# Performance work log

Measured on AMD Instinct MI355X. Metric: run time of the kernel, lower is better.

## Reference

```python
import jax, jax.numpy as jnp
import numpy as np

N = 8192
HIDDEN = 1024
PROJ = 128
T = 0.07
LN_EPS = 1e-12


def _neg_indices(n):
    # Static [n, n-2] index matrix: for row i, all j except j==i and the
    # paired sample j == (i + n//2) % n. Computed with numpy (n is static).
    half = n // 2
    idx = np.arange(n)
    mask = np.ones((n, n), dtype=bool)
    mask[idx, idx] = False
    mask[idx, (idx + half) % n] = False
    return np.nonzero(mask)[1].reshape(n, n - 2)


def setup_inputs() -> dict:
    key = jax.random.key(0)
    ks = jax.random.split(key, 3)
    scale = 1.0 / np.sqrt(HIDDEN)
    return {
        "x": jax.random.normal(ks[0], (N, HIDDEN), dtype=jnp.float32),
        "dense_w": jax.random.normal(ks[1], (HIDDEN, HIDDEN), dtype=jnp.float32) * scale,
        "dense_b": jnp.zeros((HIDDEN,), dtype=jnp.float32),
        "ln_gamma": jnp.ones((HIDDEN,), dtype=jnp.float32),
        "ln_beta": jnp.zeros((HIDDEN,), dtype=jnp.float32),
        "dec_w": jax.random.normal(ks[2], (HIDDEN, PROJ), dtype=jnp.float32) * scale,
        "dec_b": jnp.zeros((PROJ,), dtype=jnp.float32),
    }


def reference(x, dense_w, dense_b, ln_gamma, ln_beta, dec_w, dec_b):
    # dense -> gelu (exact, erf-based as in BERT) -> layernorm -> decoder
    h = x @ dense_w + dense_b
    h = jax.nn.gelu(h, approximate=False)
    mu = jnp.mean(h, axis=-1, keepdims=True)
    var = jnp.mean(jnp.square(h - mu), axis=-1, keepdims=True)
    h = (h - mu) * jax.lax.rsqrt(var + LN_EPS) * ln_gamma + ln_beta
    z = h @ dec_w + dec_b  # [N, 128]

    n = z.shape[0]
    half = n // 2
    # positive logit: dot(z_i, z_partner)
    l_pos = jnp.sum(z[:half] * z[half:], axis=-1)  # [N/2]
    l_pos = jnp.concatenate([l_pos, l_pos])[:, None]  # [N, 1]

    # full similarity matrix, then gather the N-2 negatives per row
    sims = z @ z.T  # [N, N]
    neg_idx = jnp.asarray(_neg_indices(n))  # static [N, N-2]
    l_neg = jnp.take_along_axis(sims, neg_idx, axis=1)  # [N, N-2]

    logits = jnp.concatenate([l_pos, l_neg], axis=1) / T  # [N, N-1]
    # CrossEntropyLoss with labels == 0
    loss = jnp.mean(jax.nn.logsumexp(logits, axis=-1) - logits[:, 0])
    return loss
```

## Files before the change

### kernel.cpp

```cpp
#include <hip/hip_runtime.h>
#include <math.h>
#include <stdint.h>

#define NN 8192
#define HID 1024
#define PROJ 128

constexpr float INV_T = 1.0f / 0.07f;
constexpr float LN_EPS = 1e-12f;
constexpr float CC = 14.285714285714286f * 1.4426950408889634f;

typedef __bf16 bf16x8 __attribute__((ext_vector_type(8)));
typedef float f32x4 __attribute__((ext_vector_type(4)));

#define EXP2(x) __builtin_amdgcn_exp2f(x)

#define GLD16(g, l)                                                     \
  __builtin_amdgcn_global_load_lds(                                     \
      (const __attribute__((address_space(1))) uint32_t*)(g),           \
      (__attribute__((address_space(3))) uint32_t*)(l), 16, 0, 0)

__device__ __forceinline__ uint16_t f2bf(float f) {
  union { float f; uint32_t u; } c; c.f = f;
  uint32_t r = (c.u + 0x7FFFu + ((c.u >> 16) & 1u)) >> 16;
  return (uint16_t)r;
}
__device__ __forceinline__ float bf2f(uint16_t u) {
  union { uint32_t u; float f; } c; c.u = ((uint32_t)u) << 16;
  return c.f;
}

__device__ __forceinline__ float gelu_f(float v) {
  float w = v * v;
  float u = v * fmaf(w, 0.0356774081f, 0.7978845608f);
  float e = EXP2(u * -2.8853900818f);
  return v * __builtin_amdgcn_rcpf(1.0f + e);
}

__global__ __launch_bounds__(256) void k_conv(const float* __restrict__ in,
                                              uint16_t* __restrict__ out) {
  int i = (blockIdx.x * 256 + threadIdx.x) * 4;
  float4 v = *(const float4*)(in + i);
  ushort4 o;
  o.x = f2bf(v.x); o.y = f2bf(v.y); o.z = f2bf(v.z); o.w = f2bf(v.w);
  *(ushort4*)(out + i) = o;
}

__global__ __launch_bounds__(256) void k_transpose(const float* __restrict__ in,
                                                   uint16_t* __restrict__ out,
                                                   int R, int C) {
  __shared__ uint16_t t[32][33];
  const int cb = blockIdx.x * 32, rb = blockIdx.y * 32;
  const int tr = threadIdx.x >> 3, tc4 = (threadIdx.x & 7) * 4;
  float4 v = *(const float4*)(in + (size_t)(rb + tr) * C + cb + tc4);
  t[tc4 + 0][tr] = f2bf(v.x);
  t[tc4 + 1][tr] = f2bf(v.y);
  t[tc4 + 2][tr] = f2bf(v.z);
  t[tc4 + 3][tr] = f2bf(v.w);
  __syncthreads();
  const int oc = threadIdx.x >> 3, or4 = (threadIdx.x & 7) * 4;
  ushort4 o;
  o.x = t[oc][or4 + 0]; o.y = t[oc][or4 + 1];
  o.z = t[oc][or4 + 2]; o.w = t[oc][or4 + 3];
  *(ushort4*)(out + (size_t)(cb + oc) * R + rb + or4) = o;
}

__global__ __launch_bounds__(256) void k_gemm1(
    const uint16_t* __restrict__ Ab, const uint16_t* __restrict__ Bt,
    const float* __restrict__ bias, uint16_t* __restrict__ Hout) {
  __shared__ __align__(16) uint16_t As[64 * 32];
  __shared__ __align__(16) uint16_t Bs[128 * 32];
  const int tid = threadIdx.x;
  const int bn = blockIdx.x * 128, bm = blockIdx.y * 64;
  const int wave = tid >> 6, lane = tid & 63;
  const int wx = wave & 1, wy = wave >> 1;
  const int col = lane & 15, quad = lane >> 4;
  f32x4 acc[2][4] = {};
  const char* Abase = (const char*)Ab;
  const char* Bbase = (const char*)Bt;
  for (int k0 = 0; k0 < HID; k0 += 32) {
    __syncthreads();
    {
      int off = tid * 16;
      int row = off >> 6, inner = off & 63;
      GLD16(Abase + ((size_t)(bm + row) * HID + k0) * 2 + inner,
            (char*)As + off);
    }
#pragma unroll
    for (int l = 0; l < 2; ++l) {
      int off = tid * 16 + l * 4096;
      int row = off >> 6, inner = off & 63;
      GLD16(Bbase + ((size_t)(bn + row) * HID + k0) * 2 + inner,
            (char*)Bs + off);
    }
    __syncthreads();
    bf16x8 a[2], b[4];
#pragma unroll
    for (int mt = 0; mt < 2; ++mt)
      a[mt] = *(const bf16x8*)&As[(wy * 32 + mt * 16 + col) * 32 + quad * 8];
#pragma unroll
    for (int nt = 0; nt < 4; ++nt)
      b[nt] = *(const bf16x8*)&Bs[(wx * 64 + nt * 16 + col) * 32 + quad * 8];
#pragma unroll
    for (int mt = 0; mt < 2; ++mt)
#pragma unroll
      for (int nt = 0; nt < 4; ++nt)
        acc[mt][nt] = __builtin_amdgcn_mfma_f32_16x16x32_bf16(
            a[mt], b[nt], acc[mt][nt], 0, 0, 0);
  }
#pragma unroll
  for (int nt = 0; nt < 4; ++nt) {
    int gj = bn + wx * 64 + nt * 16 + col;
    float bv = bias[gj];
#pragma unroll
    for (int mt = 0; mt < 2; ++mt)
#pragma unroll
      for (int r = 0; r < 4; ++r) {
        int gi = bm + wy * 32 + mt * 16 + quad * 4 + r;
        Hout[(size_t)gi * HID + gj] = f2bf(gelu_f(acc[mt][nt][r] + bv));
      }
  }
}

__global__ __launch_bounds__(256) void k_layernorm(
    uint16_t* __restrict__ Hm, const float* __restrict__ gamma,
    const float* __restrict__ beta) {
  const int row = blockIdx.x;
  const int tid = threadIdx.x;
  uint16_t* hr = Hm + (size_t)row * HID;
  ushort4 u = *(const ushort4*)(hr + tid * 4);
  float f0 = bf2f(u.x), f1 = bf2f(u.y), f2 = bf2f(u.z), f3 = bf2f(u.w);
  float sum = f0 + f1 + f2 + f3;
  float sq = f0 * f0 + f1 * f1 + f2 * f2 + f3 * f3;
#pragma unroll
  for (int off = 32; off > 0; off >>= 1) {
    sum += __shfl_down(sum, off);
    sq += __shfl_down(sq, off);
  }
  __shared__ float rs[4], rq[4];
  __shared__ float mu_s, rstd_s;
  const int wave = tid >> 6, lane = tid & 63;
  if (lane == 0) { rs[wave] = sum; rq[wave] = sq; }
  __syncthreads();
  if (tid == 0) {
    float s = rs[0] + rs[1] + rs[2] + rs[3];
    float q = rq[0] + rq[1] + rq[2] + rq[3];
    float mu = s * (1.0f / HID);
    float var = q * (1.0f / HID) - mu * mu;
    mu_s = mu;
    rstd_s = rsqrtf(var + LN_EPS);
  }
  __syncthreads();
  const float mu = mu_s, r = rstd_s;
  float4 g = *(const float4*)(gamma + tid * 4);
  float4 b = *(const float4*)(beta + tid * 4);
  ushort4 o;
  o.x = f2bf((f0 - mu) * r * g.x + b.x);
  o.y = f2bf((f1 - mu) * r * g.y + b.y);
  o.z = f2bf((f2 - mu) * r * g.z + b.z);
  o.w = f2bf((f3 - mu) * r * g.w + b.w);
  *(ushort4*)(hr + tid * 4) = o;
}

__global__ __launch_bounds__(256) void k_gemm2(
    const uint16_t* __restrict__ Hn, const uint16_t* __restrict__ Wt2,
    const float* __restrict__ bd, uint16_t* __restrict__ Z) {
  __shared__ __align__(16) uint16_t As2[32 * 32];
  __shared__ __align__(16) uint16_t Bs2[128 * 32];
  const int tid = threadIdx.x;
  const int bm = blockIdx.x * 32;
  const int wave = tid >> 6, lane = tid & 63;
  const int wx = wave & 1, wy = wave >> 1;
  const int col = lane & 15, quad = lane >> 4;
  f32x4 acc[4] = {};
  const char* Abase = (const char*)Hn;
  const char* Bbase = (const char*)Wt2;
  for (int k0 = 0; k0 < HID; k0 += 32) {
    __syncthreads();
    if (tid < 128) {
      int off = tid * 16;
      int row = off >> 6, inner = off & 63;
      GLD16(Abase + ((size_t)(bm + row) * HID + k0) * 2 + inner,
            (char*)As2 + off);
    }
#pragma unroll
    for (int l = 0; l < 2; ++l) {
      int off = tid * 16 + l * 4096;
      int row = off >> 6, inner = off & 63;
      GLD16(Bbase + ((size_t)row * HID + k0) * 2 + inner, (char*)Bs2 + off);
    }
    __syncthreads();
    bf16x8 a = *(const bf16x8*)&As2[(wy * 16 + col) * 32 + quad * 8];
#pragma unroll
    for (int nt = 0; nt < 4; ++nt) {
      bf16x8 b = *(const bf16x8*)&Bs2[(wx * 64 + nt * 16 + col) * 32 + quad * 8];
      acc[nt] = __builtin_amdgcn_mfma_f32_16x16x32_bf16(a, b, acc[nt], 0, 0, 0);
    }
  }
#pragma unroll
  for (int nt = 0; nt < 4; ++nt) {
    int gj = wx * 64 + nt * 16 + col;
    float bv = bd[gj];
#pragma unroll
    for (int r = 0; r < 4; ++r) {
      int gi = bm + wy * 16 + quad * 4 + r;
      Z[(size_t)gi * PROJ + gj] = f2bf(acc[nt][r] + bv);
    }
  }
}

__device__ __forceinline__ void lse_update(float& m, float& s, float v0,
                                           float v1, float v2, float v3) {
  float lm = fmaxf(fmaxf(v0, v1), fmaxf(v2, v3));
  float mn = fmaxf(m, lm);
  float t = mn * CC;
  s = s * EXP2(m * CC - t) + EXP2(v0 * CC - t) + EXP2(v1 * CC - t) +
      EXP2(v2 * CC - t) + EXP2(v3 * CC - t);
  m = mn;
}

__global__ __launch_bounds__(256) void k_sim(const uint16_t* __restrict__ Z,
                                             float* __restrict__ m_part,
                                             float* __restrict__ s_part,
                                             float* __restrict__ pos_arr) {
  __shared__ __align__(16) uint16_t Zj[128 * 136];
  const int tid = threadIdx.x;
  const int bi = blockIdx.x * 64;
  const int chunk = blockIdx.y;
  const int wave = tid >> 6, lane = tid & 63;
  const int wx = wave & 1, wy = wave >> 1;
  const int col = lane & 15, quad = lane >> 4;

  bf16x8 afr[2][4];
#pragma unroll
  for (int mt = 0; mt < 2; ++mt)
#pragma unroll
    for (int kc = 0; kc < 4; ++kc)
      afr[mt][kc] = *(const bf16x8*)(Z +
          (size_t)(bi + wy * 32 + mt * 16 + col) * PROJ + kc * 32 + quad * 8);

  float mrow[8], srow[8];
#pragma unroll
  for (int i = 0; i < 8; ++i) { mrow[i] = -INFINITY; srow[i] = 0.f; }

  const int jbase = chunk * 512;
  for (int t = 0; t < 4; ++t) {
    const int j0 = jbase + t * 128;
    __syncthreads();
#pragma unroll
    for (int l = 0; l < 8; ++l) {
      int idx = tid + l * 256;
      int row = idx >> 4, kq = (idx & 15) * 8;
      *(uint4*)&Zj[row * 136 + kq] =
          *(const uint4*)(Z + (size_t)(j0 + row) * PROJ + kq);
    }
    __syncthreads();
    f32x4 acc[2][4] = {};
#pragma unroll
    for (int kc = 0; kc < 4; ++kc) {
      bf16x8 b[4];
#pragma unroll
      for (int nt = 0; nt < 4; ++nt)
        b[nt] = *(const bf16x8*)&Zj[(wx * 64 + nt * 16 + col) * 136 +
                                    kc * 32 + quad * 8];
#pragma unroll
      for (int mt = 0; mt < 2; ++mt)
#pragma unroll
        for (int nt = 0; nt < 4; ++nt)
          acc[mt][nt] = __builtin_amdgcn_mfma_f32_16x16x32_bf16(
              afr[mt][kc], b[nt], acc[mt][nt], 0, 0, 0);
    }
    const bool is_diag = (j0 == (bi & ~127));
    const bool is_pos = (j0 == (((bi + NN / 2) & (NN - 1)) & ~127));
    if (!(is_diag || is_pos)) {
#pragma unroll
      for (int mt = 0; mt < 2; ++mt)
#pragma unroll
        for (int r = 0; r < 4; ++r)
          lse_update(mrow[mt * 4 + r], srow[mt * 4 + r], acc[mt][0][r],
                     acc[mt][1][r], acc[mt][2][r], acc[mt][3][r]);
    } else {
#pragma unroll
      for (int mt = 0; mt < 2; ++mt)
#pragma unroll
        for (int r = 0; r < 4; ++r) {
          int gi = bi + wy * 32 + mt * 16 + quad * 4 + r;
          int partner = (gi + NN / 2) & (NN - 1);
          float v[4];
#pragma unroll
          for (int nt = 0; nt < 4; ++nt) {
            int gj = j0 + wx * 64 + nt * 16 + col;
            float d = acc[mt][nt][r];
            if (is_pos && gj == partner) pos_arr[gi] = d;
            v[nt] = (is_diag && gj == gi) ? -INFINITY : d;
          }
          lse_update(mrow[mt * 4 + r], srow[mt * 4 + r], v[0], v[1], v[2],
                     v[3]);
        }
    }
  }
#pragma unroll
  for (int ri = 0; ri < 8; ++ri) {
#pragma unroll
    for (int off = 1; off < 16; off <<= 1) {
      float om = __shfl_xor(mrow[ri], off, 64);
      float os = __shfl_xor(srow[ri], off, 64);
      float mn = fmaxf(mrow[ri], om);
      float t = mn * CC;
      srow[ri] = srow[ri] * EXP2(mrow[ri] * CC - t) + os * EXP2(om * CC - t);
      mrow[ri] = mn;
    }
  }
  if (col == 0) {
    int p = chunk * 2 + wx;
#pragma unroll
    for (int ri = 0; ri < 8; ++ri) {
      int gi = bi + wy * 32 + (ri >> 2) * 16 + quad * 4 + (ri & 3);
      m_part[(size_t)p * NN + gi] = mrow[ri];
      s_part[(size_t)p * NN + gi] = srow[ri];
    }
  }
}

__global__ __launch_bounds__(256) void k_combine(
    const float* __restrict__ m_part, const float* __restrict__ s_part,
    const float* __restrict__ pos_arr, float* __restrict__ row_loss) {
  const int i = blockIdx.x * 256 + threadIdx.x;
  float M = -INFINITY;
#pragma unroll
  for (int p = 0; p < 32; ++p) M = fmaxf(M, m_part[(size_t)p * NN + i]);
  float S = 0.f;
  float t = M * CC;
#pragma unroll
  for (int p = 0; p < 32; ++p)
    S += s_part[(size_t)p * NN + i] * EXP2(m_part[(size_t)p * NN + i] * CC - t);
  row_loss[i] = (M - pos_arr[i]) * INV_T + logf(S);
}

__global__ __launch_bounds__(256) void k_final(
    const float* __restrict__ row_loss, float* __restrict__ out) {
  const int tid = threadIdx.x;
  float s = 0.f;
#pragma unroll
  for (int l = 0; l < 32; ++l) s += row_loss[tid + l * 256];
#pragma unroll
  for (int off = 32; off > 0; off >>= 1) s += __shfl_down(s, off);
  __shared__ float red[4];
  const int wave = tid >> 6, lane = tid & 63;
  if (lane == 0) red[wave] = s;
  __syncthreads();
  if (tid == 0) out[0] = (red[0] + red[1] + red[2] + red[3]) * (1.0f / NN);
}

extern "C" void kernel_launch(void* const* d_in, const int* in_sizes, int n_in,
                              void* d_out, int out_size, void* d_ws,
                              size_t ws_size, hipStream_t stream) {
  const float* x       = (const float*)d_in[0];
  const float* dense_w = (const float*)d_in[1];
  const float* dense_b = (const float*)d_in[2];
  const float* ln_g    = (const float*)d_in[3];
  const float* ln_b    = (const float*)d_in[4];
  const float* dec_w   = (const float*)d_in[5];
  const float* dec_b   = (const float*)d_in[6];
  float* out = (float*)d_out;
  char* ws = (char*)d_ws;
  uint16_t* xb = (uint16_t*)(ws);
  uint16_t* wt = (uint16_t*)(ws + 16777216);
  uint16_t* h  = (uint16_t*)(ws + 18874368);
  uint16_t* wt2     = (uint16_t*)(ws);
  uint16_t* z       = (uint16_t*)(ws + 262144);
  float*    m_part  = (float*)(ws + 2359296);
  float*    s_part  = (float*)(ws + 3407872);
  float*    pos_arr = (float*)(ws + 4456448);
  float*    row_loss= (float*)(ws + 4489216);

  k_conv<<<dim3(NN * HID / 1024), 256, 0, stream>>>(x, xb);
  k_transpose<<<dim3(32, 32), 256, 0, stream>>>(dense_w, wt, HID, HID);
  k_gemm1<<<dim3(HID / 128, NN / 64), 256, 0, stream>>>(xb, wt, dense_b, h);
  k_transpose<<<dim3(PROJ / 32, HID / 32), 256, 0, stream>>>(dec_w, wt2, HID,
                                                             PROJ);
  k_layernorm<<<dim3(NN), 256, 0, stream>>>(h, ln_g, ln_b);
  k_gemm2<<<dim3(NN / 32), 256, 0, stream>>>(h, wt2, dec_b, z);
  k_sim<<<dim3(NN / 64, 16), 256, 0, stream>>>(z, m_part, s_part, pos_arr);
  k_combine<<<dim3(NN / 256), 256, 0, stream>>>(m_part, s_part, pos_arr,
                                                row_loss);
  k_final<<<dim3(1), 256, 0, stream>>>(row_loss, out);
}
```

Baseline: 199.7 us.

## Fold layernorm into GEMM epilogues, widen GEMM1 k-step, restructure sim kernel

Removes the separate layernorm pass. GEMM1 now accumulates per-row sum and sum-of-squares with atomics, and gamma and beta are folded into the decoder weights plus a per-column correction vector, so GEMM2 applies the normalization algebraically in its epilogue. GEMM1 loads a 64-wide k slice per barrier pair, and the similarity kernel drops its LDS staging in favor of each wave reading Z tiles directly from global memory with 128 rows per block. Together these cut a full read/write pass over H and halve the partial LSE count. The trade-offs are atomics, uncached global B loads in k_sim, and some loss of precision, since normalization is applied after a bf16 GEMM on unnormalized gelu output.

```diff
diff --git a/kernel.cpp b/kernel.cpp
--- a/kernel.cpp
+++ b/kernel.cpp
@@ -38,17 +38,22 @@
 }
 
 __global__ __launch_bounds__(256) void k_conv(const float* __restrict__ in,
-                                              uint16_t* __restrict__ out) {
-  int i = (blockIdx.x * 256 + threadIdx.x) * 4;
+                                              uint16_t* __restrict__ out,
+                                              float* __restrict__ sums,
+                                              float* __restrict__ c_e) {
+  const int b = blockIdx.x, t = threadIdx.x;
+  if (b < 64) sums[b * 256 + t] = 0.f;
+  else if (b == 64) c_e[t] = 0.f;
+  int i = (b * 256 + t) * 4;
   float4 v = *(const float4*)(in + i);
   ushort4 o;
   o.x = f2bf(v.x); o.y = f2bf(v.y); o.z = f2bf(v.z); o.w = f2bf(v.w);
   *(ushort4*)(out + i) = o;
 }
 
-__global__ __launch_bounds__(256) void k_transpose(const float* __restrict__ in,
-                                                   uint16_t* __restrict__ out,
-                                                   int R, int C) {
+__global__ __launch_bounds__(256) void k_t1(const float* __restrict__ in,
+                                            uint16_t* __restrict__ out,
+                                            int R, int C) {
   __shared__ uint16_t t[32][33];
   const int cb = blockIdx.x * 32, rb = blockIdx.y * 32;
   const int tr = threadIdx.x >> 3, tc4 = (threadIdx.x & 7) * 4;
@@ -65,11 +70,42 @@
   *(ushort4*)(out + (size_t)(cb + oc) * R + rb + or4) = o;
 }
 
+__global__ __launch_bounds__(256) void k_t2(const float* __restrict__ in,
+                                            const float* __restrict__ gamma,
+                                            const float* __restrict__ beta,
+                                            uint16_t* __restrict__ out,
+                                            float* __restrict__ c_e) {
+  __shared__ float tg[32][33];
+  __shared__ float tb[32][33];
+  const int cb = blockIdx.x * 32, rb = blockIdx.y * 32;
+  const int tr = threadIdx.x >> 3, tc4 = (threadIdx.x & 7) * 4;
+  const float g = gamma[rb + tr], be = beta[rb + tr];
+  float4 v = *(const float4*)(in + (size_t)(rb + tr) * PROJ + cb + tc4);
+  tg[tc4 + 0][tr] = g * v.x;  tb[tc4 + 0][tr] = be * v.x;
+  tg[tc4 + 1][tr] = g * v.y;  tb[tc4 + 1][tr] = be * v.y;
+  tg[tc4 + 2][tr] = g * v.z;  tb[tc4 + 2][tr] = be * v.z;
+  tg[tc4 + 3][tr] = g * v.w;  tb[tc4 + 3][tr] = be * v.w;
+  __syncthreads();
+  const int oc = threadIdx.x >> 3, or4 = (threadIdx.x & 7) * 4;
+  ushort4 o;
+  o.x = f2bf(tg[oc][or4 + 0]); o.y = f2bf(tg[oc][or4 + 1]);
+  o.z = f2bf(tg[oc][or4 + 2]); o.w = f2bf(tg[oc][or4 + 3]);
+  *(ushort4*)(out + (size_t)(cb + oc) * HID + rb + or4) = o;
+  if (threadIdx.x < 32) {
+    float sc = 0.f, se = 0.f;
+#pragma unroll
+    for (int d = 0; d < 32; ++d) { sc += tg[threadIdx.x][d]; se += tb[threadIdx.x][d]; }
+    atomicAdd(c_e + cb + threadIdx.x, sc);
+    atomicAdd(c_e + 128 + cb + threadIdx.x, se);
+  }
+}
+
 __global__ __launch_bounds__(256) void k_gemm1(
     const uint16_t* __restrict__ Ab, const uint16_t* __restrict__ Bt,
-    const float* __restrict__ bias, uint16_t* __restrict__ Hout) {
-  __shared__ __align__(16) uint16_t As[64 * 32];
-  __shared__ __align__(16) uint16_t Bs[128 * 32];
+    const float* __restrict__ bias, uint16_t* __restrict__ Hout,
+    float* __restrict__ sums) {
+  __shared__ __align__(16) uint16_t As[2 * 64 * 32];
+  __shared__ __align__(16) uint16_t Bs[2 * 128 * 32];
   const int tid = threadIdx.x;
   const int bn = blockIdx.x * 128, bm = blockIdx.y * 64;
   const int wave = tid >> 6, lane = tid & 63;
@@ -78,36 +114,43 @@
   f32x4 acc[2][4] = {};
   const char* Abase = (const char*)Ab;
   const char* Bbase = (const char*)Bt;
-  for (int k0 = 0; k0 < HID; k0 += 32) {
+  for (int k0 = 0; k0 < HID; k0 += 64) {
     __syncthreads();
-    {
-      int off = tid * 16;
-      int row = off >> 6, inner = off & 63;
-      GLD16(Abase + ((size_t)(bm + row) * HID + k0) * 2 + inner,
-            (char*)As + off);
-    }
 #pragma unroll
     for (int l = 0; l < 2; ++l) {
       int off = tid * 16 + l * 4096;
-      int row = off >> 6, inner = off & 63;
-      GLD16(Bbase + ((size_t)(bn + row) * HID + k0) * 2 + inner,
+      int h = off >> 12, row = (off >> 6) & 63, inner = off & 63;
+      GLD16(Abase + ((size_t)(bm + row) * HID + k0 + h * 32) * 2 + inner,
+            (char*)As + off);
+    }
+#pragma unroll
+    for (int l = 0; l < 4; ++l) {
+      int off = tid * 16 + l * 4096;
+      int h = off >> 13, row = (off >> 6) & 127, inner = off & 63;
+      GLD16(Bbase + ((size_t)(bn + row) * HID + k0 + h * 32) * 2 + inner,
             (char*)Bs + off);
     }
     __syncthreads();
-    bf16x8 a[2], b[4];
-#pragma unroll
-    for (int mt = 0; mt < 2; ++mt)
-      a[mt] = *(const bf16x8*)&As[(wy * 32 + mt * 16 + col) * 32 + quad * 8];
-#pragma unroll
-    for (int nt = 0; nt < 4; ++nt)
-      b[nt] = *(const bf16x8*)&Bs[(wx * 64 + nt * 16 + col) * 32 + quad * 8];
-#pragma unroll
-    for (int mt = 0; mt < 2; ++mt)
+#pragma unroll
+    for (int h = 0; h < 2; ++h) {
+      bf16x8 a[2], b[4];
+#pragma unroll
+      for (int mt = 0; mt < 2; ++mt)
+        a[mt] = *(const bf16x8*)&As[h * 2048 +
+                                    (wy * 32 + mt * 16 + col) * 32 + quad * 8];
 #pragma unroll
       for (int nt = 0; nt < 4; ++nt)
-        acc[mt][nt] = __builtin_amdgcn_mfma_f32_16x16x32_bf16(
-            a[mt], b[nt], acc[mt][nt], 0, 0, 0);
-  }
+        b[nt] = *(const bf16x8*)&Bs[h * 4096 +
+                                    (wx * 64 + nt * 16 + col) * 32 + quad * 8];
+#pragma unroll
+      for (int mt = 0; mt < 2; ++mt)
+#pragma unroll
+        for (int nt = 0; nt < 4; ++nt)
+          acc[mt][nt] = __builtin_amdgcn_mfma_f32_16x16x32_bf16(
+              a[mt], b[nt], acc[mt][nt], 0, 0, 0);
+    }
+  }
+  float rsum[2][4] = {}, rsq[2][4] = {};
 #pragma unroll
   for (int nt = 0; nt < 4; ++nt) {
     int gj = bn + wx * 64 + nt * 16 + col;
@@ -117,63 +160,51 @@
 #pragma unroll
       for (int r = 0; r < 4; ++r) {
         int gi = bm + wy * 32 + mt * 16 + quad * 4 + r;
-        Hout[(size_t)gi * HID + gj] = f2bf(gelu_f(acc[mt][nt][r] + bv));
+        float gl = gelu_f(acc[mt][nt][r] + bv);
+        Hout[(size_t)gi * HID + gj] = f2bf(gl);
+        rsum[mt][r] += gl;
+        rsq[mt][r] = fmaf(gl, gl, rsq[mt][r]);
       }
   }
-}
-
-__global__ __launch_bounds__(256) void k_layernorm(
-    uint16_t* __restrict__ Hm, const float* __restrict__ gamma,
-    const float* __restrict__ beta) {
-  const int row = blockIdx.x;
-  const int tid = threadIdx.x;
-  uint16_t* hr = Hm + (size_t)row * HID;
-  ushort4 u = *(const ushort4*)(hr + tid * 4);
-  float f0 = bf2f(u.x), f1 = bf2f(u.y), f2 = bf2f(u.z), f3 = bf2f(u.w);
-  float sum = f0 + f1 + f2 + f3;
-  float sq = f0 * f0 + f1 * f1 + f2 * f2 + f3 * f3;
-#pragma unroll
-  for (int off = 32; off > 0; off >>= 1) {
-    sum += __shfl_down(sum, off);
-    sq += __shfl_down(sq, off);
-  }
-  __shared__ float rs[4], rq[4];
-  __shared__ float mu_s, rstd_s;
-  const int wave = tid >> 6, lane = tid & 63;
-  if (lane == 0) { rs[wave] = sum; rq[wave] = sq; }
-  __syncthreads();
-  if (tid == 0) {
-    float s = rs[0] + rs[1] + rs[2] + rs[3];
-    float q = rq[0] + rq[1] + rq[2] + rq[3];
-    float mu = s * (1.0f / HID);
-    float var = q * (1.0f / HID) - mu * mu;
-    mu_s = mu;
-    rstd_s = rsqrtf(var + LN_EPS);
-  }
-  __syncthreads();
-  const float mu = mu_s, r = rstd_s;
-  float4 g = *(const float4*)(gamma + tid * 4);
-  float4 b = *(const float4*)(beta + tid * 4);
-  ushort4 o;
-  o.x = f2bf((f0 - mu) * r * g.x + b.x);
-  o.y = f2bf((f1 - mu) * r * g.y + b.y);
-  o.z = f2bf((f2 - mu) * r * g.z + b.z);
-  o.w = f2bf((f3 - mu) * r * g.w + b.w);
-  *(ushort4*)(hr + tid * 4) = o;
+#pragma unroll
+  for (int mt = 0; mt < 2; ++mt)
+#pragma unroll
+    for (int r = 0; r < 4; ++r) {
+      float s1 = rsum[mt][r], s2 = rsq[mt][r];
+#pragma unroll
+      for (int off = 1; off < 16; off <<= 1) {
+        s1 += __shfl_xor(s1, off, 64);
+        s2 += __shfl_xor(s2, off, 64);
+      }
+      if (col == 0) {
+        int gi = bm + wy * 32 + mt * 16 + quad * 4 + r;
+        atomicAdd(&sums[gi], s1);
+        atomicAdd(&sums[NN + gi], s2);
+      }
+    }
 }
 
 __global__ __launch_bounds__(256) void k_gemm2(
-    const uint16_t* __restrict__ Hn, const uint16_t* __restrict__ Wt2,
-    const float* __restrict__ bd, uint16_t* __restrict__ Z) {
+    const uint16_t* __restrict__ Hb, const uint16_t* __restrict__ Wt2,
+    const float* __restrict__ bd, const float* __restrict__ sums,
+    const float* __restrict__ c_e, uint16_t* __restrict__ Z) {
   __shared__ __align__(16) uint16_t As2[32 * 32];
   __shared__ __align__(16) uint16_t Bs2[128 * 32];
+  __shared__ float muS[32], rS[32];
   const int tid = threadIdx.x;
   const int bm = blockIdx.x * 32;
   const int wave = tid >> 6, lane = tid & 63;
   const int wx = wave & 1, wy = wave >> 1;
   const int col = lane & 15, quad = lane >> 4;
+  if (tid < 32) {
+    float s = sums[bm + tid], q = sums[NN + bm + tid];
+    float mu = s * (1.0f / HID);
+    float var = q * (1.0f / HID) - mu * mu;
+    muS[tid] = mu;
+    rS[tid] = rsqrtf(var + LN_EPS);
+  }
   f32x4 acc[4] = {};
-  const char* Abase = (const char*)Hn;
+  const char* Abase = (const char*)Hb;
   const char* Bbase = (const char*)Wt2;
   for (int k0 = 0; k0 < HID; k0 += 32) {
     __syncthreads();
@@ -200,22 +231,26 @@
 #pragma unroll
   for (int nt = 0; nt < 4; ++nt) {
     int gj = wx * 64 + nt * 16 + col;
-    float bv = bd[gj];
+    float ck = c_e[gj], ek = c_e[128 + gj] + bd[gj];
 #pragma unroll
     for (int r = 0; r < 4; ++r) {
-      int gi = bm + wy * 16 + quad * 4 + r;
-      Z[(size_t)gi * PROJ + gj] = f2bf(acc[nt][r] + bv);
-    }
-  }
-}
-
-__device__ __forceinline__ void lse_update(float& m, float& s, float v0,
-                                           float v1, float v2, float v3) {
+      int li = wy * 16 + quad * 4 + r;
+      float mu = muS[li], rr = rS[li];
+      float z = fmaf(rr, acc[nt][r], fmaf(-rr * mu, ck, ek));
+      Z[(size_t)(bm + li) * PROJ + gj] = f2bf(z);
+    }
+  }
+}
+
+__device__ __forceinline__ void lse4(float& m, float& s, float v0, float v1,
+                                     float v2, float v3) {
   float lm = fmaxf(fmaxf(v0, v1), fmaxf(v2, v3));
   float mn = fmaxf(m, lm);
-  float t = mn * CC;
-  s = s * EXP2(m * CC - t) + EXP2(v0 * CC - t) + EXP2(v1 * CC - t) +
-      EXP2(v2 * CC - t) + EXP2(v3 * CC - t);
+  float tn = mn * CC;
+  float rs = EXP2(fmaf(m, CC, -tn));
+  float e = EXP2(fmaf(v0, CC, -tn)) + EXP2(fmaf(v1, CC, -tn)) +
+            EXP2(fmaf(v2, CC, -tn)) + EXP2(fmaf(v3, CC, -tn));
+  s = fmaf(s, rs, e);
   m = mn;
 }
 
@@ -223,46 +258,34 @@
                                              float* __restrict__ m_part,
                                              float* __restrict__ s_part,
                                              float* __restrict__ pos_arr) {
-  __shared__ __align__(16) uint16_t Zj[128 * 136];
   const int tid = threadIdx.x;
-  const int bi = blockIdx.x * 64;
+  const int wave = tid >> 6, lane = tid & 63;
+  const int col = lane & 15, quad = lane >> 4;
+  const int wrow0 = blockIdx.x * 128 + wave * 32;
   const int chunk = blockIdx.y;
-  const int wave = tid >> 6, lane = tid & 63;
-  const int wx = wave & 1, wy = wave >> 1;
-  const int col = lane & 15, quad = lane >> 4;
-
   bf16x8 afr[2][4];
 #pragma unroll
   for (int mt = 0; mt < 2; ++mt)
 #pragma unroll
     for (int kc = 0; kc < 4; ++kc)
       afr[mt][kc] = *(const bf16x8*)(Z +
-          (size_t)(bi + wy * 32 + mt * 16 + col) * PROJ + kc * 32 + quad * 8);
-
-  float mrow[8], srow[8];
-#pragma unroll
-  for (int i = 0; i < 8; ++i) { mrow[i] = -INFINITY; srow[i] = 0.f; }
-
+          (size_t)(wrow0 + mt * 16 + col) * PROJ + kc * 32 + quad * 8);
+  float ms[8], ss[8];
+#pragma unroll
+  for (int i = 0; i < 8; ++i) { ms[i] = -INFINITY; ss[i] = 0.f; }
+  const int diag_t = wrow0 & ~63;
+  const int pos_t = ((wrow0 + NN / 2) & (NN - 1)) & ~63;
   const int jbase = chunk * 512;
-  for (int t = 0; t < 4; ++t) {
-    const int j0 = jbase + t * 128;
-    __syncthreads();
-#pragma unroll
-    for (int l = 0; l < 8; ++l) {
-      int idx = tid + l * 256;
-      int row = idx >> 4, kq = (idx & 15) * 8;
-      *(uint4*)&Zj[row * 136 + kq] =
-          *(const uint4*)(Z + (size_t)(j0 + row) * PROJ + kq);
-    }
-    __syncthreads();
+  for (int t8 = 0; t8 < 8; ++t8) {
+    const int jt = jbase + t8 * 64;
     f32x4 acc[2][4] = {};
 #pragma unroll
     for (int kc = 0; kc < 4; ++kc) {
       bf16x8 b[4];
 #pragma unroll
       for (int nt = 0; nt < 4; ++nt)
-        b[nt] = *(const bf16x8*)&Zj[(wx * 64 + nt * 16 + col) * 136 +
-                                    kc * 32 + quad * 8];
+        b[nt] = *(const bf16x8*)(Z + (size_t)(jt + nt * 16 + col) * PROJ +
+                                 kc * 32 + quad * 8);
 #pragma unroll
       for (int mt = 0; mt < 2; ++mt)
 #pragma unroll
@@ -270,32 +293,30 @@
           acc[mt][nt] = __builtin_amdgcn_mfma_f32_16x16x32_bf16(
               afr[mt][kc], b[nt], acc[mt][nt], 0, 0, 0);
     }
-    const bool is_diag = (j0 == (bi & ~127));
-    const bool is_pos = (j0 == (((bi + NN / 2) & (NN - 1)) & ~127));
-    if (!(is_diag || is_pos)) {
+    if (jt != diag_t && jt != pos_t) {
 #pragma unroll
       for (int mt = 0; mt < 2; ++mt)
 #pragma unroll
         for (int r = 0; r < 4; ++r)
-          lse_update(mrow[mt * 4 + r], srow[mt * 4 + r], acc[mt][0][r],
-                     acc[mt][1][r], acc[mt][2][r], acc[mt][3][r]);
+          lse4(ms[mt * 4 + r], ss[mt * 4 + r], acc[mt][0][r], acc[mt][1][r],
+               acc[mt][2][r], acc[mt][3][r]);
     } else {
+      const bool isd = (jt == diag_t);
 #pragma unroll
       for (int mt = 0; mt < 2; ++mt)
 #pragma unroll
         for (int r = 0; r < 4; ++r) {
-          int gi = bi + wy * 32 + mt * 16 + quad * 4 + r;
+          int gi = wrow0 + mt * 16 + quad * 4 + r;
           int partner = (gi + NN / 2) & (NN - 1);
           float v[4];
 #pragma unroll
           for (int nt = 0; nt < 4; ++nt) {
-            int gj = j0 + wx * 64 + nt * 16 + col;
+            int gj = jt + nt * 16 + col;
             float d = acc[mt][nt][r];
-            if (is_pos && gj == partner) pos_arr[gi] = d;
-            v[nt] = (is_diag && gj == gi) ? -INFINITY : d;
+            if (!isd && gj == partner) pos_arr[gi] = d;
+            v[nt] = (isd && gj == gi) ? -INFINITY : d;
           }
-          lse_update(mrow[mt * 4 + r], srow[mt * 4 + r], v[0], v[1], v[2],
-                     v[3]);
+          lse4(ms[mt * 4 + r], ss[mt * 4 + r], v[0], v[1], v[2], v[3]);
         }
     }
   }
@@ -303,21 +324,21 @@
   for (int ri = 0; ri < 8; ++ri) {
 #pragma unroll
     for (int off = 1; off < 16; off <<= 1) {
-      float om = __shfl_xor(mrow[ri], off, 64);
-      float os = __shfl_xor(srow[ri], off, 64);
-      float mn = fmaxf(mrow[ri], om);
-      float t = mn * CC;
-      srow[ri] = srow[ri] * EXP2(mrow[ri] * CC - t) + os * EXP2(om * CC - t);
-      mrow[ri] = mn;
+      float om = __shfl_xor(ms[ri], off, 64);
+      float os = __shfl_xor(ss[ri], off, 64);
+      float mn = fmaxf(ms[ri], om);
+      float tn = mn * CC;
+      ss[ri] = fmaf(ss[ri], EXP2(fmaf(ms[ri], CC, -tn)),
+                    os * EXP2(fmaf(om, CC, -tn)));
+      ms[ri] = mn;
     }
   }
   if (col == 0) {
-    int p = chunk * 2 + wx;
 #pragma unroll
     for (int ri = 0; ri < 8; ++ri) {
-      int gi = bi + wy * 32 + (ri >> 2) * 16 + quad * 4 + (ri & 3);
-      m_part[(size_t)p * NN + gi] = mrow[ri];
-      s_part[(size_t)p * NN + gi] = srow[ri];
+      int gi = wrow0 + (ri >> 2) * 16 + quad * 4 + (ri & 3);
+      m_part[(size_t)chunk * NN + gi] = ms[ri];
+      s_part[(size_t)chunk * NN + gi] = ss[ri];
     }
   }
 }
@@ -328,12 +349,12 @@
   const int i = blockIdx.x * 256 + threadIdx.x;
   float M = -INFINITY;
 #pragma unroll
-  for (int p = 0; p < 32; ++p) M = fmaxf(M, m_part[(size_t)p * NN + i]);
+  for (int p = 0; p < 16; ++p) M = fmaxf(M, m_part[(size_t)p * NN + i]);
   float S = 0.f;
   float t = M * CC;
 #pragma unroll
-  for (int p = 0; p < 32; ++p)
-    S += s_part[(size_t)p * NN + i] * EXP2(m_part[(size_t)p * NN + i] * CC - t);
+  for (int p = 0; p < 16; ++p)
+    S += s_part[(size_t)p * NN + i] * EXP2(fmaf(m_part[(size_t)p * NN + i], CC, -t));
   row_loss[i] = (M - pos_arr[i]) * INV_T + logf(S);
 }
 
@@ -364,24 +385,25 @@
   const float* dec_b   = (const float*)d_in[6];
   float* out = (float*)d_out;
   char* ws = (char*)d_ws;
-  uint16_t* xb = (uint16_t*)(ws);
-  uint16_t* wt = (uint16_t*)(ws + 16777216);
-  uint16_t* h  = (uint16_t*)(ws + 18874368);
-  uint16_t* wt2     = (uint16_t*)(ws);
-  uint16_t* z       = (uint16_t*)(ws + 262144);
-  float*    m_part  = (float*)(ws + 2359296);
-  float*    s_part  = (float*)(ws + 3407872);
-  float*    pos_arr = (float*)(ws + 4456448);
-  float*    row_loss= (float*)(ws + 4489216);
-
-  k_conv<<<dim3(NN * HID / 1024), 256, 0, stream>>>(x, xb);
-  k_transpose<<<dim3(32, 32), 256, 0, stream>>>(dense_w, wt, HID, HID);
-  k_gemm1<<<dim3(HID / 128, NN / 64), 256, 0, stream>>>(xb, wt, dense_b, h);
-  k_transpose<<<dim3(PROJ / 32, HID / 32), 256, 0, stream>>>(dec_w, wt2, HID,
-                                                             PROJ);
-  k_layernorm<<<dim3(NN), 256, 0, stream>>>(h, ln_g, ln_b);
-  k_gemm2<<<dim3(NN / 32), 256, 0, stream>>>(h, wt2, dec_b, z);
-  k_sim<<<dim3(NN / 64, 16), 256, 0, stream>>>(z, m_part, s_part, pos_arr);
+  uint16_t* xb      = (uint16_t*)(ws);
+  uint16_t* wt      = (uint16_t*)(ws + 16777216);
+  uint16_t* h       = (uint16_t*)(ws + 18874368);
+  uint16_t* z       = (uint16_t*)(ws);
+  float*    m_part  = (float*)(ws + 16777216);
+  float*    s_part  = (float*)(ws + 17301504);
+  uint16_t* wt2     = (uint16_t*)(ws + 35651584);
+  float*    sums    = (float*)(ws + 35913728);
+  float*    c_e     = (float*)(ws + 35979264);
+  float*    pos_arr = (float*)(ws + 35980288);
+  float*    row_loss= (float*)(ws + 36013056);
+
+  k_conv<<<dim3(NN * HID / 1024), 256, 0, stream>>>(x, xb, sums, c_e);
+  k_t1<<<dim3(32, 32), 256, 0, stream>>>(dense_w, wt, HID, HID);
+  k_t2<<<dim3(PROJ / 32, HID / 32), 256, 0, stream>>>(dec_w, ln_g, ln_b, wt2,
+                                                      c_e);
+  k_gemm1<<<dim3(8, 128), 256, 0, stream>>>(xb, wt, dense_b, h, sums);
+  k_gemm2<<<dim3(NN / 32), 256, 0, stream>>>(h, wt2, dec_b, sums, c_e, z);
+  k_sim<<<dim3(64, 16), 256, 0, stream>>>(z, m_part, s_part, pos_arr);
   k_combine<<<dim3(NN / 256), 256, 0, stream>>>(m_part, s_part, pos_arr,
                                                 row_loss);
   k_final<<<dim3(1), 256, 0, stream>>>(row_loss, out);
```

After: 213.8 us. 1.07x slower.
